# Kernel optimization log

Hardware: AMD Instinct MI355X
Metric: run time of the kernel (lower is better)

## Reference

```python
import jax, jax.numpy as jnp
import numpy as np

B, C, H, W = 4, 256, 64, 64
GROUPS = 32
EPS = 1e-6
N_BITS_QKV = 8
N_BITS_SM = 8


def setup_inputs() -> dict:
    key = jax.random.key(0)
    ks = jax.random.split(key, 6)
    s = 1.0 / np.sqrt(C)
    return {
        "x": jax.random.normal(ks[0], (B, C, H, W), jnp.float32),
        "gn_scale": jnp.ones((C,), jnp.float32),
        "gn_bias": jnp.zeros((C,), jnp.float32),
        "wq": jax.random.normal(ks[1], (C, C), jnp.float32) * s,
        "bq": jnp.zeros((C,), jnp.float32),
        "wk": jax.random.normal(ks[2], (C, C), jnp.float32) * s,
        "bk": jnp.zeros((C,), jnp.float32),
        "wv": jax.random.normal(ks[3], (C, C), jnp.float32) * s,
        "bv": jnp.zeros((C,), jnp.float32),
        "wproj": jax.random.normal(ks[4], (C, C), jnp.float32) * s,
        "bproj": jnp.zeros((C,), jnp.float32),
        # per-tensor uniform-affine quantizer params (delta, zero_point)
        "dq": jnp.float32(8.0 / 255.0), "zq": jnp.float32(128.0),
        "dk": jnp.float32(8.0 / 255.0), "zk": jnp.float32(128.0),
        "dv": jnp.float32(8.0 / 255.0), "zv": jnp.float32(128.0),
        "dw": jnp.float32(1.0 / 255.0), "zw": jnp.float32(0.0),
    }


def ste_round(x):
    # round with straight-through gradient (as in round_ste of BRECQ/QDrop)
    return x + jax.lax.stop_gradient(jnp.round(x) - x)


def fake_quant(x, delta, zero_point, n_bits):
    # UniformAffineQuantizer: quant -> clamp -> dequant
    n_levels = 2 ** n_bits
    x_int = ste_round(x / delta) + zero_point
    x_q = jnp.clip(x_int, 0, n_levels - 1)
    return (x_q - zero_point) * delta


def group_norm(x, scale, bias):
    b, c, h, w = x.shape
    xg = x.reshape(b, GROUPS, (c // GROUPS) * h * w)
    mu = xg.mean(-1, keepdims=True)
    var = xg.var(-1, keepdims=True)
    xn = ((xg - mu) * jax.lax.rsqrt(var + EPS)).reshape(b, c, h, w)
    return xn * scale[None, :, None, None] + bias[None, :, None, None]


def conv1x1(x, w, b):
    # 1x1 conv == channel-mixing matmul
    return jnp.einsum('bchw,oc->bohw', x, w) + b[None, :, None, None]


def reference(x, gn_scale, gn_bias, wq, bq, wk, bk, wv, bv, wproj, bproj,
              dq, zq, dk, zk, dv, zv, dw, zw):
    h_ = group_norm(x, gn_scale, gn_bias)
    q = conv1x1(h_, wq, bq)
    k = conv1x1(h_, wk, bk)
    v = conv1x1(h_, wv, bv)
    b, c, h, w = q.shape
    hw = h * w
    q = q.reshape(b, c, hw).transpose(0, 2, 1)   # [b, hw, c]
    k = k.reshape(b, c, hw)                      # [b, c, hw]
    q = fake_quant(q, dq, zq, N_BITS_QKV)
    k = fake_quant(k, dk, zk, N_BITS_QKV)
    attn = jnp.einsum('bnc,bcm->bnm', q, k) * (c ** -0.5)  # [b, hw, hw]
    attn = jax.nn.softmax(attn, axis=2)
    v = fake_quant(v.reshape(b, c, hw), dv, zv, N_BITS_QKV)
    attn = fake_quant(attn.transpose(0, 2, 1), dw, zw, N_BITS_SM)  # [b, m, n]
    h_out = jnp.einsum('bcm,bmn->bcn', v, attn).reshape(b, c, h, w)
    return x + conv1x1(h_out, wproj, bproj)
```

## Files before the change

### kernel.cpp

```cpp
#include <hip/hip_runtime.h>


#define Bb 4
#define Cc 256
#define Nn 4096
#define NGRP 32
#define LOG2E 1.4426950408889634f

typedef unsigned short u16;
typedef unsigned int   u32;
typedef unsigned char  u8;
typedef __attribute__((ext_vector_type(8))) short bf16x8;
typedef __attribute__((ext_vector_type(4))) float f32x4;
typedef __attribute__((ext_vector_type(4))) int   i32x4;

#define MFMA16(a,b,c)    __builtin_amdgcn_mfma_f32_16x16x32_bf16((a),(b),(c),0,0,0)
#define MFMA_I8(a,b,c)   __builtin_amdgcn_mfma_i32_16x16x64_i8((a),(b),(c),0,0,0)
#define EXP2F(x)         __builtin_amdgcn_exp2f(x)

static __device__ __forceinline__ u16 f2bf(float x){
  u32 u = __float_as_uint(x);
  u += 0x7fffu + ((u >> 16) & 1u);
  return (u16)(u >> 16);
}
static __device__ __forceinline__ float bf2f(u16 h){ return __uint_as_float(((u32)h) << 16); }

union U64c { u16 u[4]; uint2 v; };

__global__ __launch_bounds__(256) void k_gn_stats(const float* __restrict__ x,
                                                  float* __restrict__ mu, float* __restrict__ rs){
  int bg = blockIdx.x;
  const float4* p = (const float4*)(x + (size_t)bg * (8 * Nn));
  float s = 0.f, q = 0.f;
  for (int i = threadIdx.x; i < 8*Nn/4; i += 256){
    float4 v = p[i];
    s += v.x + v.y + v.z + v.w;
    q += v.x*v.x + v.y*v.y + v.z*v.z + v.w*v.w;
  }
  __shared__ float rsum[256], rsq[256];
  rsum[threadIdx.x] = s; rsq[threadIdx.x] = q;
  __syncthreads();
  for (int off = 128; off > 0; off >>= 1){
    if (threadIdx.x < off){ rsum[threadIdx.x] += rsum[threadIdx.x+off]; rsq[threadIdx.x] += rsq[threadIdx.x+off]; }
    __syncthreads();
  }
  if (threadIdx.x == 0){
    const float inv = 1.0f / (8*Nn);
    float m = rsum[0]*inv;
    float var = rsq[0]*inv - m*m;
    mu[bg] = m; rs[bg] = rsqrtf(var + 1e-6f);
  }
}

__global__ __launch_bounds__(256) void k_wsplit(const float* __restrict__ wq, const float* __restrict__ wk,
                                                const float* __restrict__ wv, const float* __restrict__ wp,
                                                u16* __restrict__ WH, u16* __restrict__ WL){
  int gid = blockIdx.x*256 + threadIdx.x;
  int mat = gid >> 16, idx = gid & 65535;
  const float* src = (mat == 0) ? wq : (mat == 1) ? wk : (mat == 2) ? wv : wp;
  float w = src[idx];
  u16 h = f2bf(w);
  WH[gid] = h;
  WL[gid] = f2bf(w - bf2f(h));
}

__global__ __launch_bounds__(256) void k_gn_apply(const float* __restrict__ x,
                                                  const float* __restrict__ gsc, const float* __restrict__ gbi,
                                                  const float* __restrict__ mu, const float* __restrict__ rs,
                                                  u16* __restrict__ hhi, u16* __restrict__ hlo){
  int nt = blockIdx.x, ct = blockIdx.y, b = blockIdx.z;
  int n0 = nt*64, c0 = ct*64;
  __shared__ float yt[64*65];
  __shared__ float sa[64], sb[64];
  int t = threadIdx.x;
  if (t < 64){
    int c = c0 + t;
    int bg = b*NGRP + (c >> 3);
    float a = rs[bg] * gsc[c];
    sa[t] = a;
    sb[t] = gbi[c] - mu[bg]*a;
  }
  __syncthreads();
  #pragma unroll
  for (int j = 0; j < 4; ++j){
    int id = t + j*256;
    int r = id >> 4, cq = id & 15;
    float4 v = *(const float4*)(x + ((size_t)b*Cc + c0 + r)*Nn + n0 + cq*4);
    float a = sa[r], bb = sb[r];
    yt[r*65 + cq*4 + 0] = v.x*a + bb;
    yt[r*65 + cq*4 + 1] = v.y*a + bb;
    yt[r*65 + cq*4 + 2] = v.z*a + bb;
    yt[r*65 + cq*4 + 3] = v.w*a + bb;
  }
  __syncthreads();
  int nl = t >> 2, cg = (t & 3) * 16;
  size_t base = ((size_t)b*Nn + n0 + nl)*Cc + c0 + cg;
  #pragma unroll
  for (int half = 0; half < 2; ++half){
    union { u16 u[8]; uint4 v; } Ph, Pl;
    #pragma unroll
    for (int u = 0; u < 8; ++u){
      float y = yt[(cg + half*8 + u)*65 + nl];
      u16 h = f2bf(y);
      Ph.u[u] = h; Pl.u[u] = f2bf(y - bf2f(h));
    }
    *(uint4*)(hhi + base + half*8) = Ph.v;
    *(uint4*)(hlo + base + half*8) = Pl.v;
  }
}

__global__ __launch_bounds__(256) void k_convqkv(const u16* __restrict__ WH, const u16* __restrict__ WL,
                                                 const u16* __restrict__ Hhi, const u16* __restrict__ Hlo,
                                                 const float* __restrict__ bq, const float* __restrict__ bk,
                                                 const float* __restrict__ bv,
                                                 const float* __restrict__ dq, const float* __restrict__ zq,
                                                 const float* __restrict__ dk, const float* __restrict__ zk,
                                                 const float* __restrict__ dv, const float* __restrict__ zv,
                                                 u8* __restrict__ qT8, u8* __restrict__ kT8,
                                                 u8* __restrict__ v8){
  int nt = blockIdx.x, ot = blockIdx.y, b = blockIdx.z;
  __shared__ u16 Lh[64*256], Ll[64*256];
  int t = threadIdx.x, lane = t & 63, wave = t >> 6;
  int lo16 = lane & 15, quad = lane >> 4;
  int o0 = ot*64 + wave*16;

  {
    const u16* hb = Hhi + ((size_t)b*Nn + nt*64) * 256;
    const u16* lb = Hlo + ((size_t)b*Nn + nt*64) * 256;
    #pragma unroll
    for (int j = 0; j < 8; ++j){
      int id = t + j*256;
      int r = id >> 5, ch = id & 31;
      int sw = (ch ^ (r & 15)) * 8;
      *(uint4*)(Lh + r*256 + sw) = *(const uint4*)(hb + (size_t)r*256 + ch*8);
      *(uint4*)(Ll + r*256 + sw) = *(const uint4*)(lb + (size_t)r*256 + ch*8);
    }
  }
  __syncthreads();

  const float* Bs[3] = {bq, bk, bv};
  const float* Dsr[3] = {dq, dk, dv};
  const float* Zs[3] = {zq, zk, zv};

  #pragma unroll
  for (int ws = 0; ws < 3; ++ws){
    bf16x8 awh[8], awl[8];
    {
      const u16* wbh = WH + (size_t)ws*65536 + (size_t)(o0 + lo16) * 256 + quad*8;
      const u16* wbl = WL + (size_t)ws*65536 + (size_t)(o0 + lo16) * 256 + quad*8;
      #pragma unroll
      for (int k = 0; k < 8; ++k){
        awh[k] = *(const bf16x8*)(wbh + k*32);
        awl[k] = *(const bf16x8*)(wbl + k*32);
      }
    }
    f32x4 zf = {0.f,0.f,0.f,0.f};
    f32x4 acc[4] = {zf, zf, zf, zf};
    #pragma unroll
    for (int k = 0; k < 8; ++k){
      #pragma unroll
      for (int ns = 0; ns < 4; ++ns){
        int r = ns*16 + lo16;
        int ph = ((k*4 + quad) ^ (r & 15)) * 8;
        bf16x8 bh = *(const bf16x8*)(Lh + r*256 + ph);
        bf16x8 bl = *(const bf16x8*)(Ll + r*256 + ph);
        acc[ns] = MFMA16(awh[k], bh, acc[ns]);
        acc[ns] = MFMA16(awl[k], bh, acc[ns]);
        acc[ns] = MFMA16(awh[k], bl, acc[ns]);
      }
    }
    float bia[4];
    #pragma unroll
    for (int r = 0; r < 4; ++r) bia[r] = Bs[ws][o0 + quad*4 + r];
    float z = Zs[ws][0]; float invd = 1.0f / Dsr[ws][0];

    if (ws < 2){
      u8* outT = (ws == 0) ? qT8 : kT8;
      #pragma unroll
      for (int ns = 0; ns < 4; ++ns){
        int n = nt*64 + ns*16 + lo16;
        u32 w = 0;
        #pragma unroll
        for (int r = 0; r < 4; ++r){
          float v = acc[ns][r] + bia[r];
          float xq = fminf(fmaxf(rintf(v*invd) + z, 0.f), 255.f);
          int qi = (int)rintf(xq - z);
          w |= ((u32)(qi & 255)) << (8*r);
        }
        *(u32*)(outT + ((size_t)b*Nn + n)*Cc + o0 + quad*4) = w;
      }
    } else {
      #pragma unroll
      for (int ns = 0; ns < 4; ++ns){
        int n = nt*64 + ns*16 + lo16;
        #pragma unroll
        for (int r = 0; r < 4; ++r){
          float v = acc[ns][r] + bia[r];
          float xq = fminf(fmaxf(rintf(v*invd) + z, 0.f), 255.f);
          int qi = (int)rintf(xq - z);
          v8[((size_t)b*Cc + o0 + quad*4 + r)*Nn + n] = (u8)(qi & 255);
        }
      }
    }
  }
}

__global__ __launch_bounds__(256) void k_conv(const u16* __restrict__ WH, const u16* __restrict__ WL,
                                              const u16* __restrict__ Hh,
                                              const float* __restrict__ bias,
                                              const float* __restrict__ xres, float* __restrict__ outF){
  int nt = blockIdx.x, ot = blockIdx.y, b = blockIdx.z;
  __shared__ u16 Lh[64*128];
  int t = threadIdx.x, lane = t & 63, wave = t >> 6;
  int lo16 = lane & 15, quad = lane >> 4;
  int o0 = ot*64 + wave*16;

  bf16x8 awh[8], awl[8];
  {
    const u16* wbh = WH + (size_t)3*65536 + (size_t)(o0 + lo16) * 256 + quad*8;
    const u16* wbl = WL + (size_t)3*65536 + (size_t)(o0 + lo16) * 256 + quad*8;
    #pragma unroll
    for (int k = 0; k < 8; ++k){
      awh[k] = *(const bf16x8*)(wbh + k*32);
      awl[k] = *(const bf16x8*)(wbl + k*32);
    }
  }
  f32x4 zf = {0.f,0.f,0.f,0.f};
  f32x4 acc[4] = {zf, zf, zf, zf};

  const u16* hb = Hh + ((size_t)b*Nn + nt*64) * 256;
  for (int kc = 0; kc < 2; ++kc){
    __syncthreads();
    for (int id = t; id < 64*16; id += 256){
      int r = id >> 4, ch = id & 15;
      int sw = (ch ^ (r & 7)) * 8;
      *(uint4*)(Lh + r*128 + sw) = *(const uint4*)(hb + (size_t)r*256 + kc*128 + ch*8);
    }
    __syncthreads();
    #pragma unroll
    for (int k4 = 0; k4 < 4; ++k4){
      int k = kc*4 + k4;
      #pragma unroll
      for (int ns = 0; ns < 4; ++ns){
        int r = ns*16 + lo16;
        int ch = ((k4*4 + quad) ^ (r & 7)) * 8;
        bf16x8 bh = *(const bf16x8*)(Lh + r*128 + ch);
        acc[ns] = MFMA16(awh[k], bh, acc[ns]);
        acc[ns] = MFMA16(awl[k], bh, acc[ns]);
      }
    }
  }

  float bia[4];
  #pragma unroll
  for (int r = 0; r < 4; ++r) bia[r] = bias[o0 + quad*4 + r];
  #pragma unroll
  for (int ns = 0; ns < 4; ++ns){
    int n = nt*64 + ns*16 + lo16;
    #pragma unroll
    for (int r = 0; r < 4; ++r){
      size_t a = ((size_t)b*Cc + o0 + quad*4 + r)*Nn + n;
      outF[a] = xres[a] + acc[ns][r] + bia[r];
    }
  }
}

static __device__ __forceinline__ int sq4(u32 w){
  int s = 0;
  #pragma unroll
  for (int j = 0; j < 4; ++j){ int v = (int)((signed char)((w >> (8*j)) & 0xffu)); s += v*v; }
  return s;
}
static __device__ __forceinline__ int ssum4(u32 w){
  return ((int)(w << 24) >> 24) + ((int)(w << 16) >> 24) + ((int)(w << 8) >> 24) + ((int)w >> 24);
}
__global__ __launch_bounds__(256) void k_normvs(const u8* __restrict__ qT8, const u8* __restrict__ kT8,
                                                const u8* __restrict__ v8,
                                                u32* __restrict__ stat, int* __restrict__ vsum){
  if (blockIdx.x < 128){
    int gid = blockIdx.x*256 + threadIdx.x;
    int which = gid >> 14;
    int rid = gid & 16383;
    const u8* row = (which ? kT8 : qT8) + (size_t)rid * 256;
    u32 acc = 0;
    const uint4* p = (const uint4*)row;
    #pragma unroll
    for (int i = 0; i < 16; ++i){
      uint4 w = p[i];
      acc += (u32)(sq4(w.x) + sq4(w.y) + sq4(w.z) + sq4(w.w));
    }
    #pragma unroll
    for (int msk = 32; msk > 0; msk >>= 1){
      u32 o = (u32)__shfl_xor((int)acc, msk, 64);
      acc = acc > o ? acc : o;
    }
    if ((threadIdx.x & 63) == 0)
      atomicMax(&stat[which*4 + (rid >> 12)], acc);
  } else {
    int row = blockIdx.x - 128;
    uint4 w = *(const uint4*)(v8 + (size_t)row*Nn + threadIdx.x*16);
    int s = ssum4(w.x) + ssum4(w.y) + ssum4(w.z) + ssum4(w.w);
    #pragma unroll
    for (int msk = 1; msk < 64; msk <<= 1) s += __shfl_xor(s, msk, 64);
    __shared__ int r4[4];
    if ((threadIdx.x & 63) == 0) r4[threadIdx.x >> 6] = s;
    __syncthreads();
    if (threadIdx.x == 0) vsum[row] = r4[0] + r4[1] + r4[2] + r4[3];
  }
}

__global__ __launch_bounds__(1024) void k_qpv(const u8* __restrict__ qT8, const u8* __restrict__ kT8,
                                              const u8* __restrict__ v8,
                                              const u32* __restrict__ stat,
                                              const float* __restrict__ pdq, const float* __restrict__ pdk,
                                              const float* __restrict__ pdw, const float* __restrict__ pzw,
                                              const int* __restrict__ vsum,
                                              const float* __restrict__ pdv,
                                              u16* __restrict__ h2){
  int nt = blockIdx.x, b = blockIdx.y;
  __shared__ alignas(16) u8  Kt[2][2][64*256];
  __shared__ alignas(16) u32 Pt[2][2][64*16];
  __shared__ float Lbuf[4][4][16];
  int t = threadIdx.x, lane = t & 63, w = t >> 6;
  int lo16 = lane & 15, q = lane >> 4;
  int ms = w & 3, nsq = w >> 2;

  float sc2 = pdq[0]*pdk[0]*0.0625f*LOG2E;
  float M2 = sc2 * sqrtf((float)stat[b] * (float)stat[4+b]);
  float zw = pzw[0];

  i32x4 qf[4];
  {
    const u8* qb = qT8 + ((size_t)b*Nn + nt*64 + nsq*16 + lo16)*256;
    #pragma unroll
    for (int kk = 0; kk < 4; ++kk)
      qf[kk] = *(const i32x4*)(qb + kk*64 + q*16);
  }

  int krow = t >> 4, kch = t & 15;
  int kdst = krow*256 + ((kch ^ (krow & 15)) << 4);
  const u8* kb = kT8 + (size_t)b*Nn*256;

  int mrow = ms*16 + lo16;
  int kofs[4];
  #pragma unroll
  for (int kk = 0; kk < 4; ++kk) kofs[kk] = mrow*256 + (((kk*4 + q) ^ (mrow & 15)) << 4);

  const u8* vp = v8 + ((size_t)(b*Cc + w*16 + lo16))*Nn + q*16;

  float lr = 0.f;
  {
    const u8* kld = kb + (size_t)krow*256 + kch*16;
    uint4 kr0 = *(const uint4*)(kld);
    uint4 kr1 = *(const uint4*)(kld + 16384);
    *(uint4*)(Kt[0][0] + kdst) = kr0;
    *(uint4*)(Kt[0][1] + kdst) = kr1;
    kld += 2*16384;
    kr0 = *(const uint4*)(kld);
    kr1 = *(const uint4*)(kld + 16384);
    kld += 2*16384;
    __syncthreads();
    i32x4 spA0, spB0, spA1, spB1;
    #pragma unroll 2
    for (int i = 0; i < 32; ++i){
      int cur = i & 1;
      i32x4 sA0 = {0,0,0,0}, sB0 = {0,0,0,0}, sA1 = {0,0,0,0}, sB1 = {0,0,0,0};
      sA0 = MFMA_I8(*(const i32x4*)(Kt[cur][0] + kofs[0]), qf[0], sA0);
      sB0 = MFMA_I8(*(const i32x4*)(Kt[cur][0] + kofs[1]), qf[1], sB0);
      sA1 = MFMA_I8(*(const i32x4*)(Kt[cur][1] + kofs[0]), qf[0], sA1);
      sB1 = MFMA_I8(*(const i32x4*)(Kt[cur][1] + kofs[1]), qf[1], sB1);
      sA0 = MFMA_I8(*(const i32x4*)(Kt[cur][0] + kofs[2]), qf[2], sA0);
      sB0 = MFMA_I8(*(const i32x4*)(Kt[cur][0] + kofs[3]), qf[3], sB0);
      sA1 = MFMA_I8(*(const i32x4*)(Kt[cur][1] + kofs[2]), qf[2], sA1);
      sB1 = MFMA_I8(*(const i32x4*)(Kt[cur][1] + kofs[3]), qf[3], sB1);
      if (i < 31){
        *(uint4*)(Kt[cur ^ 1][0] + kdst) = kr0;
        *(uint4*)(Kt[cur ^ 1][1] + kdst) = kr1;
        if (i < 30){
          kr0 = *(const uint4*)(kld);
          kr1 = *(const uint4*)(kld + 16384);
          kld += 2*16384;
        }
      }
      if (i > 0){
        #pragma unroll
        for (int r = 0; r < 4; ++r){
          lr += EXP2F(fmaf((float)(spA0[r] + spB0[r]), sc2, -M2));
          lr += EXP2F(fmaf((float)(spA1[r] + spB1[r]), sc2, -M2));
        }
      }
      spA0 = sA0; spB0 = sB0; spA1 = sA1; spB1 = sB1;
      __syncthreads();
    }
    #pragma unroll
    for (int r = 0; r < 4; ++r){
      lr += EXP2F(fmaf((float)(spA0[r] + spB0[r]), sc2, -M2));
      lr += EXP2F(fmaf((float)(spA1[r] + spB1[r]), sc2, -M2));
    }
  }
  lr += __shfl_xor(lr, 16, 64);
  lr += __shfl_xor(lr, 32, 64);
  if (lane < 16) Lbuf[nsq][ms][lo16] = lr;
  __syncthreads();
  float Ls = Lbuf[nsq][0][lo16] + Lbuf[nsq][1][lo16] + Lbuf[nsq][2][lo16] + Lbuf[nsq][3][lo16];
  float crn = __log2f(1.0f / (pdw[0] * Ls)) - M2;

  i32x4 zi = {0,0,0,0};
  i32x4 acc[4] = {zi,zi,zi,zi};
  int nrow = nsq*16 + lo16;
  int pdst = nrow*16 + ((ms ^ (nrow & 3) ^ ((nrow >> 2) & 3)) << 2) + q;
  int pofs[4];
  #pragma unroll
  for (int ns = 0; ns < 4; ++ns){
    int pr = ns*16 + lo16;
    pofs[ns] = pr*16 + ((q ^ (pr & 3) ^ ((pr >> 2) & 3)) << 2);
  }
  {
    const u8* kld = kb + (size_t)krow*256 + kch*16;
    uint4 kr0 = *(const uint4*)(kld);
    uint4 kr1 = *(const uint4*)(kld + 16384);
    *(uint4*)(Kt[0][0] + kdst) = kr0;
    *(uint4*)(Kt[0][1] + kdst) = kr1;
    kld += 2*16384;
    kr0 = *(const uint4*)(kld);
    kr1 = *(const uint4*)(kld + 16384);
    kld += 2*16384;
    const u8* vld = vp + 128;
    i32x4 af0 = *(const i32x4*)(vp);
    i32x4 af1 = *(const i32x4*)(vp + 64);
    i32x4 af0p, af1p, af0pp, af1pp;
    i32x4 spA0, spB0, spA1, spB1;
    __syncthreads();
    #pragma unroll 2
    for (int i = 0; i < 32; ++i){
      int cur = i & 1;
      i32x4 sA0 = {0,0,0,0}, sB0 = {0,0,0,0}, sA1 = {0,0,0,0}, sB1 = {0,0,0,0};
      sA0 = MFMA_I8(*(const i32x4*)(Kt[cur][0] + kofs[0]), qf[0], sA0);
      sB0 = MFMA_I8(*(const i32x4*)(Kt[cur][0] + kofs[1]), qf[1], sB0);
      sA1 = MFMA_I8(*(const i32x4*)(Kt[cur][1] + kofs[0]), qf[0], sA1);
      sB1 = MFMA_I8(*(const i32x4*)(Kt[cur][1] + kofs[1]), qf[1], sB1);
      sA0 = MFMA_I8(*(const i32x4*)(Kt[cur][0] + kofs[2]), qf[2], sA0);
      sB0 = MFMA_I8(*(const i32x4*)(Kt[cur][0] + kofs[3]), qf[3], sB0);
      sA1 = MFMA_I8(*(const i32x4*)(Kt[cur][1] + kofs[2]), qf[2], sA1);
      sB1 = MFMA_I8(*(const i32x4*)(Kt[cur][1] + kofs[3]), qf[3], sB1);
      if (i < 31){
        *(uint4*)(Kt[cur ^ 1][0] + kdst) = kr0;
        *(uint4*)(Kt[cur ^ 1][1] + kdst) = kr1;
        if (i < 30){
          kr0 = *(const uint4*)(kld);
          kr1 = *(const uint4*)(kld + 16384);
          kld += 2*16384;
        }
      }
      if (i > 1){
        acc[0] = MFMA_I8(af0pp, *(const i32x4*)(Pt[cur][0] + pofs[0]), acc[0]);
        acc[1] = MFMA_I8(af0pp, *(const i32x4*)(Pt[cur][0] + pofs[1]), acc[1]);
        acc[2] = MFMA_I8(af0pp, *(const i32x4*)(Pt[cur][0] + pofs[2]), acc[2]);
        acc[3] = MFMA_I8(af0pp, *(const i32x4*)(Pt[cur][0] + pofs[3]), acc[3]);
        acc[0] = MFMA_I8(af1pp, *(const i32x4*)(Pt[cur][1] + pofs[0]), acc[0]);
        acc[1] = MFMA_I8(af1pp, *(const i32x4*)(Pt[cur][1] + pofs[1]), acc[1]);
        acc[2] = MFMA_I8(af1pp, *(const i32x4*)(Pt[cur][1] + pofs[2]), acc[2]);
        acc[3] = MFMA_I8(af1pp, *(const i32x4*)(Pt[cur][1] + pofs[3]), acc[3]);
      }
      if (i > 0){
        u32 wp0 = 0, wp1 = 0;
        #pragma unroll
        for (int r = 0; r < 4; ++r){
          float at0 = EXP2F(fmaf((float)(spA0[r] + spB0[r]), sc2, crn));
          float y0 = fminf(fmaxf(rintf(at0) + zw, 0.f), 255.f);
          wp0 = __builtin_amdgcn_cvt_pk_u8_f32(y0, (u32)r, wp0);
          float at1 = EXP2F(fmaf((float)(spA1[r] + spB1[r]), sc2, crn));
          float y1 = fminf(fmaxf(rintf(at1) + zw, 0.f), 255.f);
          wp1 = __builtin_amdgcn_cvt_pk_u8_f32(y1, (u32)r, wp1);
        }
        Pt[cur ^ 1][0][pdst] = wp0 ^ 0x80808080u;
        Pt[cur ^ 1][1][pdst] = wp1 ^ 0x80808080u;
      }
      spA0 = sA0; spB0 = sB0; spA1 = sA1; spB1 = sB1;
      af0pp = af0p; af0p = af0; af1pp = af1p; af1p = af1;
      if (i < 31){
        af0 = *(const i32x4*)(vld);
        af1 = *(const i32x4*)(vld + 64);
        vld += 128;
      }
      __syncthreads();
    }
    acc[0] = MFMA_I8(af0pp, *(const i32x4*)(Pt[0][0] + pofs[0]), acc[0]);
    acc[1] = MFMA_I8(af0pp, *(const i32x4*)(Pt[0][0] + pofs[1]), acc[1]);
    acc[2] = MFMA_I8(af0pp, *(const i32x4*)(Pt[0][0] + pofs[2]), acc[2]);
    acc[3] = MFMA_I8(af0pp, *(const i32x4*)(Pt[0][0] + pofs[3]), acc[3]);
    acc[0] = MFMA_I8(af1pp, *(const i32x4*)(Pt[0][1] + pofs[0]), acc[0]);
    acc[1] = MFMA_I8(af1pp, *(const i32x4*)(Pt[0][1] + pofs[1]), acc[1]);
    acc[2] = MFMA_I8(af1pp, *(const i32x4*)(Pt[0][1] + pofs[2]), acc[2]);
    acc[3] = MFMA_I8(af1pp, *(const i32x4*)(Pt[0][1] + pofs[3]), acc[3]);
    {
      u32 wp0 = 0, wp1 = 0;
      #pragma unroll
      for (int r = 0; r < 4; ++r){
        float at0 = EXP2F(fmaf((float)(spA0[r] + spB0[r]), sc2, crn));
        float y0 = fminf(fmaxf(rintf(at0) + zw, 0.f), 255.f);
        wp0 = __builtin_amdgcn_cvt_pk_u8_f32(y0, (u32)r, wp0);
        float at1 = EXP2F(fmaf((float)(spA1[r] + spB1[r]), sc2, crn));
        float y1 = fminf(fmaxf(rintf(at1) + zw, 0.f), 255.f);
        wp1 = __builtin_amdgcn_cvt_pk_u8_f32(y1, (u32)r, wp1);
      }
      Pt[1][0][pdst] = wp0 ^ 0x80808080u;
      Pt[1][1][pdst] = wp1 ^ 0x80808080u;
    }
    __syncthreads();
    acc[0] = MFMA_I8(af0p, *(const i32x4*)(Pt[1][0] + pofs[0]), acc[0]);
    acc[1] = MFMA_I8(af0p, *(const i32x4*)(Pt[1][0] + pofs[1]), acc[1]);
    acc[2] = MFMA_I8(af0p, *(const i32x4*)(Pt[1][0] + pofs[2]), acc[2]);
    acc[3] = MFMA_I8(af0p, *(const i32x4*)(Pt[1][0] + pofs[3]), acc[3]);
    acc[0] = MFMA_I8(af1p, *(const i32x4*)(Pt[1][1] + pofs[0]), acc[0]);
    acc[1] = MFMA_I8(af1p, *(const i32x4*)(Pt[1][1] + pofs[1]), acc[1]);
    acc[2] = MFMA_I8(af1p, *(const i32x4*)(Pt[1][1] + pofs[2]), acc[2]);
    acc[3] = MFMA_I8(af1p, *(const i32x4*)(Pt[1][1] + pofs[3]), acc[3]);
  }

  float s = pdv[0] * pdw[0];
  float corr = s * (128.0f - zw);
  int c0 = w*16 + q*4;
  float cv[4];
  #pragma unroll
  for (int r = 0; r < 4; ++r) cv[r] = corr * (float)vsum[b*Cc + c0 + r];
  #pragma unroll
  for (int ns = 0; ns < 4; ++ns){
    int n = nt*64 + ns*16 + lo16;
    U64c Uh;
    #pragma unroll
    for (int r = 0; r < 4; ++r)
      Uh.u[r] = f2bf(s*(float)acc[ns][r] + cv[r]);
    *(uint2*)(h2 + ((size_t)b*Nn + n)*Cc + c0) = Uh.v;
  }
}

extern "C" void kernel_launch(void* const* d_in, const int* in_sizes, int n_in,
                              void* d_out, int out_size, void* d_ws, size_t ws_size,
                              hipStream_t stream){
  (void)in_sizes; (void)n_in; (void)out_size; (void)ws_size;
  const float* x   = (const float*)d_in[0];
  const float* gsc = (const float*)d_in[1];
  const float* gbi = (const float*)d_in[2];
  const float* wq  = (const float*)d_in[3];
  const float* bq  = (const float*)d_in[4];
  const float* wk  = (const float*)d_in[5];
  const float* bk  = (const float*)d_in[6];
  const float* wv  = (const float*)d_in[7];
  const float* bv  = (const float*)d_in[8];
  const float* wp  = (const float*)d_in[9];
  const float* bp  = (const float*)d_in[10];
  const float* dq  = (const float*)d_in[11];
  const float* zq  = (const float*)d_in[12];
  const float* dk  = (const float*)d_in[13];
  const float* zk  = (const float*)d_in[14];
  const float* dv  = (const float*)d_in[15];
  const float* zv  = (const float*)d_in[16];
  const float* dw  = (const float*)d_in[17];
  const float* zw  = (const float*)d_in[18];
  float* out = (float*)d_out;

  const size_t SZT = (size_t)Bb*Nn*Cc;
  u16* hT_hi = (u16*)d_ws;
  u16* hT_lo = hT_hi + SZT;
  u16* h2    = hT_lo + SZT;
  u8*  qT8   = (u8*)(h2 + SZT);
  u8*  kT8   = qT8 + SZT;
  u8*  v8    = kT8 + SZT;
  u16* WH    = (u16*)(v8 + SZT);
  u16* WL    = WH + 4*65536;
  float* mu  = (float*)(WL + 4*65536);
  float* rs  = mu + 128;
  u32*  stat = (u32*)(rs + 128);
  int*  vsum = (int*)(stat + 8);

  k_gn_stats<<<dim3(Bb*NGRP), 256, 0, stream>>>(x, mu, rs);
  k_wsplit<<<dim3(1024), 256, 0, stream>>>(wq, wk, wv, wp, WH, WL);
  k_gn_apply<<<dim3(Nn/64, Cc/64, Bb), 256, 0, stream>>>(x, gsc, gbi, mu, rs, hT_hi, hT_lo);

  k_convqkv<<<dim3(Nn/64, 4, Bb), 256, 0, stream>>>(WH, WL, hT_hi, hT_lo,
                                                    bq, bk, bv, dq, zq, dk, zk, dv, zv,
                                                    qT8, kT8, v8);

  hipMemsetAsync(stat, 0, 8*sizeof(u32), stream);
  k_normvs<<<dim3(128 + Bb*Cc), 256, 0, stream>>>(qT8, kT8, v8, stat, vsum);

  k_qpv<<<dim3(Nn/64, Bb), 1024, 0, stream>>>(qT8, kT8, v8, stat, dq, dk, dw, zw, vsum, dv, h2);

  k_conv<<<dim3(Nn/64, 4, Bb), 256, 0, stream>>>(WH, WL, h2, bp, x, out);
}
```

Measured before the change: 246.2 us.

## Fuse output projection conv into attention kernel epilogue via shared memory

```diff
diff --git a/kernel.cpp b/kernel.cpp
--- a/kernel.cpp
+++ b/kernel.cpp
@@ -205,66 +205,6 @@
   }
 }
 
-__global__ __launch_bounds__(256) void k_conv(const u16* __restrict__ WH, const u16* __restrict__ WL,
-                                              const u16* __restrict__ Hh,
-                                              const float* __restrict__ bias,
-                                              const float* __restrict__ xres, float* __restrict__ outF){
-  int nt = blockIdx.x, ot = blockIdx.y, b = blockIdx.z;
-  __shared__ u16 Lh[64*128];
-  int t = threadIdx.x, lane = t & 63, wave = t >> 6;
-  int lo16 = lane & 15, quad = lane >> 4;
-  int o0 = ot*64 + wave*16;
-
-  bf16x8 awh[8], awl[8];
-  {
-    const u16* wbh = WH + (size_t)3*65536 + (size_t)(o0 + lo16) * 256 + quad*8;
-    const u16* wbl = WL + (size_t)3*65536 + (size_t)(o0 + lo16) * 256 + quad*8;
-    #pragma unroll
-    for (int k = 0; k < 8; ++k){
-      awh[k] = *(const bf16x8*)(wbh + k*32);
-      awl[k] = *(const bf16x8*)(wbl + k*32);
-    }
-  }
-  f32x4 zf = {0.f,0.f,0.f,0.f};
-  f32x4 acc[4] = {zf, zf, zf, zf};
-
-  const u16* hb = Hh + ((size_t)b*Nn + nt*64) * 256;
-  for (int kc = 0; kc < 2; ++kc){
-    __syncthreads();
-    for (int id = t; id < 64*16; id += 256){
-      int r = id >> 4, ch = id & 15;
-      int sw = (ch ^ (r & 7)) * 8;
-      *(uint4*)(Lh + r*128 + sw) = *(const uint4*)(hb + (size_t)r*256 + kc*128 + ch*8);
-    }
-    __syncthreads();
-    #pragma unroll
-    for (int k4 = 0; k4 < 4; ++k4){
-      int k = kc*4 + k4;
-      #pragma unroll
-      for (int ns = 0; ns < 4; ++ns){
-        int r = ns*16 + lo16;
-        int ch = ((k4*4 + quad) ^ (r & 7)) * 8;
-        bf16x8 bh = *(const bf16x8*)(Lh + r*128 + ch);
-        acc[ns] = MFMA16(awh[k], bh, acc[ns]);
-        acc[ns] = MFMA16(awl[k], bh, acc[ns]);
-      }
-    }
-  }
-
-  float bia[4];
-  #pragma unroll
-  for (int r = 0; r < 4; ++r) bia[r] = bias[o0 + quad*4 + r];
-  #pragma unroll
-  for (int ns = 0; ns < 4; ++ns){
-    int n = nt*64 + ns*16 + lo16;
-    #pragma unroll
-    for (int r = 0; r < 4; ++r){
-      size_t a = ((size_t)b*Cc + o0 + quad*4 + r)*Nn + n;
-      outF[a] = xres[a] + acc[ns][r] + bia[r];
-    }
-  }
-}
-
 static __device__ __forceinline__ int sq4(u32 w){
   int s = 0;
   #pragma unroll
@@ -316,7 +256,10 @@
                                               const float* __restrict__ pdw, const float* __restrict__ pzw,
                                               const int* __restrict__ vsum,
                                               const float* __restrict__ pdv,
-                                              u16* __restrict__ h2){
+                                              const u16* __restrict__ WH, const u16* __restrict__ WL,
+                                              const float* __restrict__ bp,
+                                              const float* __restrict__ xres,
+                                              float* __restrict__ outF){
   int nt = blockIdx.x, b = blockIdx.y;
   __shared__ alignas(16) u8  Kt[2][2][64*256];
   __shared__ alignas(16) u32 Pt[2][2][64*16];
@@ -518,20 +461,64 @@
     acc[3] = MFMA_I8(af1p, *(const i32x4*)(Pt[1][1] + pofs[3]), acc[3]);
   }
 
-  float s = pdv[0] * pdw[0];
-  float corr = s * (128.0f - zw);
-  int c0 = w*16 + q*4;
-  float cv[4];
-  #pragma unroll
-  for (int r = 0; r < 4; ++r) cv[r] = corr * (float)vsum[b*Cc + c0 + r];
-  #pragma unroll
-  for (int ns = 0; ns < 4; ++ns){
-    int n = nt*64 + ns*16 + lo16;
-    U64c Uh;
-    #pragma unroll
-    for (int r = 0; r < 4; ++r)
-      Uh.u[r] = f2bf(s*(float)acc[ns][r] + cv[r]);
-    *(uint2*)(h2 + ((size_t)b*Nn + n)*Cc + c0) = Uh.v;
+  u16* Ht = (u16*)Kt;
+  {
+    float s = pdv[0] * pdw[0];
+    float corr = s * (128.0f - zw);
+    int c0 = w*16 + q*4;
+    int kc0 = c0 >> 7;
+    int ch8 = (c0 >> 3) & 15;
+    int c4  = c0 & 7;
+    float cv[4];
+    #pragma unroll
+    for (int r = 0; r < 4; ++r) cv[r] = corr * (float)vsum[b*Cc + c0 + r];
+    #pragma unroll
+    for (int ns = 0; ns < 4; ++ns){
+      int rrow = ns*16 + lo16;
+      U64c Uh;
+      #pragma unroll
+      for (int r = 0; r < 4; ++r)
+        Uh.u[r] = f2bf(s*(float)acc[ns][r] + cv[r]);
+      *(uint2*)(Ht + rrow*256 + kc0*128 + ((ch8 ^ (rrow & 7)) << 3) + c4) = Uh.v;
+    }
+  }
+  __syncthreads();
+  {
+    f32x4 zf = {0.f,0.f,0.f,0.f};
+    f32x4 acc2[4] = {zf, zf, zf, zf};
+    const u16* wbh = WH + (size_t)3*65536 + (size_t)(w*16 + lo16)*256 + q*8;
+    const u16* wbl = WL + (size_t)3*65536 + (size_t)(w*16 + lo16)*256 + q*8;
+    #pragma unroll
+    for (int kc = 0; kc < 2; ++kc){
+      bf16x8 ah[4], al[4];
+      #pragma unroll
+      for (int k4 = 0; k4 < 4; ++k4){
+        ah[k4] = *(const bf16x8*)(wbh + kc*128 + k4*32);
+        al[k4] = *(const bf16x8*)(wbl + kc*128 + k4*32);
+      }
+      #pragma unroll
+      for (int k4 = 0; k4 < 4; ++k4){
+        #pragma unroll
+        for (int ns = 0; ns < 4; ++ns){
+          int rrow = ns*16 + lo16;
+          bf16x8 bh = *(const bf16x8*)(Ht + rrow*256 + kc*128 + (((k4*4 + q) ^ (rrow & 7)) << 3));
+          acc2[ns] = MFMA16(ah[k4], bh, acc2[ns]);
+          acc2[ns] = MFMA16(al[k4], bh, acc2[ns]);
+        }
+      }
+    }
+    float bia[4];
+    #pragma unroll
+    for (int r = 0; r < 4; ++r) bia[r] = bp[w*16 + q*4 + r];
+    #pragma unroll
+    for (int ns = 0; ns < 4; ++ns){
+      int n = nt*64 + ns*16 + lo16;
+      #pragma unroll
+      for (int r = 0; r < 4; ++r){
+        size_t a = ((size_t)b*Cc + w*16 + q*4 + r)*Nn + n;
+        outF[a] = xres[a] + acc2[ns][r] + bia[r];
+      }
+    }
   }
 }
 
@@ -585,7 +572,6 @@
   hipMemsetAsync(stat, 0, 8*sizeof(u32), stream);
   k_normvs<<<dim3(128 + Bb*Cc), 256, 0, stream>>>(qT8, kT8, v8, stat, vsum);
 
-  k_qpv<<<dim3(Nn/64, Bb), 1024, 0, stream>>>(qT8, kT8, v8, stat, dq, dk, dw, zw, vsum, dv, h2);
-
-  k_conv<<<dim3(Nn/64, 4, Bb), 256, 0, stream>>>(WH, WL, h2, bp, x, out);
-}
+  k_qpv<<<dim3(Nn/64, Bb), 1024, 0, stream>>>(qT8, kT8, v8, stat, dq, dk, dw, zw, vsum, dv,
+                                              WH, WL, bp, x, out);
+}
```

After: 240.1 us. 2.5% less time.
